# Performance work log

Measured on AMD Instinct MI355X. Metric: run time of the kernel, lower is better.

The kernel has to match this reference:

```python
import jax, jax.numpy as jnp
import numpy as np

C = 256
RED = 8
D = C // RED  # qk dim = 32
EPS = 1e-5   # nn.LayerNorm default


def setup_inputs() -> dict:
    key = jax.random.key(0)
    ks = jax.random.split(key, 10)
    B, H, W = 4, 64, 64
    s = 0.02
    return {
        "x": jax.random.normal(ks[0], (B, C, H, W), dtype=jnp.float32),
        "wq": jax.random.normal(ks[1], (D, C), dtype=jnp.float32) * s,
        "bq": jax.random.normal(ks[2], (D,), dtype=jnp.float32) * s,
        "wk": jax.random.normal(ks[3], (D, C), dtype=jnp.float32) * s,
        "bk": jax.random.normal(ks[4], (D,), dtype=jnp.float32) * s,
        "wv": jax.random.normal(ks[5], (C, C), dtype=jnp.float32) * s,
        "bv": jax.random.normal(ks[6], (C,), dtype=jnp.float32) * s,
        "gamma": jax.random.normal(ks[7], (1,), dtype=jnp.float32) * 0.1,
        "ln_w": jnp.ones((C,), dtype=jnp.float32),
        "ln_b": jnp.zeros((C,), dtype=jnp.float32),
    }


def reference(x, wq, bq, wk, bk, wv, bv, gamma, ln_w, ln_b):
    B, Cc, H, W = x.shape
    N = H * W
    xf = x.reshape(B, Cc, N)  # [B,C,N]
    # 1x1 convs == per-pixel linear over channels
    q = jnp.einsum('dc,bcn->bnd', wq, xf) + bq              # [B,N,D]
    k = jnp.einsum('dc,bcn->bdn', wk, xf) + bk[:, None]     # [B,D,N]
    v = jnp.einsum('ec,bcn->ben', wv, xf) + bv[:, None]     # [B,C,N]
    scale = 1.0 / (D ** 0.5)
    scores = jnp.einsum('bnd,bdm->bnm', q, k) * scale       # [B,N,N]
    # original subtracts row max then softmax; jax.nn.softmax is equivalent & stable
    attn = jax.nn.softmax(scores, axis=-1)                  # [B,N,N]
    out = jnp.einsum('bcm,bnm->bcn', v, attn)               # [B,C,N]
    res = gamma[0] * out + xf                               # gamma residual
    # LayerNorm over channel dim (module permutes to channels-last)
    r = res.transpose(0, 2, 1)                              # [B,N,C]
    mu = jnp.mean(r, axis=-1, keepdims=True)
    var = jnp.mean(jnp.square(r - mu), axis=-1, keepdims=True)
    y = (r - mu) * jax.lax.rsqrt(var + EPS) * ln_w + ln_b
    return y.transpose(0, 2, 1).reshape(B, Cc, H, W)
```

## Files before the change

kernel.cpp:

```cpp
#include <hip/hip_runtime.h>
#include <hip/hip_bf16.h>

#define NPIX 4096
#define NCH  256

typedef __attribute__((ext_vector_type(8))) short short8;
typedef __attribute__((ext_vector_type(16))) float f32x16;
typedef __attribute__((ext_vector_type(2))) unsigned int u32x2;

__device__ inline unsigned short bfbits(float f) {
    __hip_bfloat16 h = __float2bfloat16(f);
    return *reinterpret_cast<unsigned short*>(&h);
}

__device__ inline unsigned int pkfp8x4(float a, float b, float c, float d) {
    int w = __builtin_amdgcn_cvt_pk_fp8_f32(a, b, 0, false);
    w = __builtin_amdgcn_cvt_pk_fp8_f32(c, d, w, true);
    return (unsigned int)w;
}

__device__ inline unsigned char fp8b(float a) {
    return (unsigned char)(__builtin_amdgcn_cvt_pk_fp8_f32(a, a, 0, false) & 0xff);
}

__device__ inline float bperm(int srclane, float v) {
    return __int_as_float(__builtin_amdgcn_ds_bpermute(
        srclane << 2, __float_as_int(v)));
}

__global__ void __launch_bounds__(256) prep_kernel(
    const float* __restrict__ x,
    const float* __restrict__ wq, const float* __restrict__ bq,
    const float* __restrict__ wk, const float* __restrict__ bk,
    const float* __restrict__ wv, const float* __restrict__ bv,
    __hip_bfloat16* __restrict__ Wc, float* __restrict__ bc,
    __hip_bfloat16* __restrict__ XTg)
{
    const int bid = blockIdx.x;
    const int t   = threadIdx.x;
    if (bid >= 1024) {
        const int j = bid - 1024;
        const float kQ = 0.17677669529663687f * 1.4426950408889634f;
        const float* src;
        float sc = 1.0f;
        if (j < 32)       { src = wq + j * 256; }
        else if (j < 64)  { src = wk + (j - 32) * 256; sc = kQ; }
        else              { src = wv + (j - 64) * 256; }
        Wc[j * 256 + t] = __float2bfloat16(src[t] * sc);
        if (t == 0) {
            float bb = (j < 32) ? bq[j] : (j < 64) ? bk[j - 32] * kQ : bv[j - 64];
            bc[j] = bb;
        }
        return;
    }
    __shared__ float xs[64][65];
    const int b  = bid >> 8;
    const int c0 = ((bid >> 6) & 3) * 64;
    const int n0 = (bid & 63) * 64;
    const float* xb = x + ((size_t)b * NCH + c0) * NPIX + n0;
    #pragma unroll 4
    for (int i = 0; i < 16; ++i) {
        int c = i * 4 + (t >> 6);
        int n = t & 63;
        xs[c][n] = xb[(size_t)c * NPIX + n];
    }
    __syncthreads();
    #pragma unroll 4
    for (int i = 0; i < 16; ++i) {
        int nn = i * 4 + (t >> 6);
        int cL = t & 63;
        XTg[((size_t)b * NPIX + n0 + nn) * NCH + c0 + cL] =
            __float2bfloat16(xs[cL][nn]);
    }
}

__global__ void __launch_bounds__(256) proj_kernel(
    const __hip_bfloat16* __restrict__ Wc, const float* __restrict__ bc,
    const __hip_bfloat16* __restrict__ XTg,
    unsigned char* __restrict__ Q8, unsigned char* __restrict__ K8,
    unsigned char* __restrict__ V8)
{
    const int b    = blockIdx.z;
    const int t    = threadIdx.x;
    const int lane = t & 63;
    const int wid  = t >> 6;
    const int lo   = lane & 31;
    const int hi   = lane >> 5;
    const int n0   = blockIdx.x * 128 + wid * 32;
    const int jb   = blockIdx.y * 5;

    short8 xf[16];
    const __hip_bfloat16* xr = XTg + ((size_t)b * NPIX + n0 + lo) * NCH;
    #pragma unroll
    for (int ks = 0; ks < 16; ++ks)
        xf[ks] = *(const short8*)(xr + ks * 16 + hi * 8);

    for (int jo = 0; jo < 5; ++jo) {
        const int jt = jb + jo;
        f32x16 acc;
        #pragma unroll
        for (int r = 0; r < 16; ++r) acc[r] = 0.f;
        const __hip_bfloat16* wr = Wc + (size_t)(jt * 32 + lo) * NCH;
        #pragma unroll
        for (int ks = 0; ks < 16; ++ks) {
            short8 wf = *(const short8*)(wr + ks * 16 + hi * 8);
            acc = __builtin_amdgcn_mfma_f32_32x32x16_bf16(wf, xf[ks], acc, 0, 0, 0);
        }
        if (jt < 2) {
            unsigned char* dst = (jt == 0 ? Q8 : K8)
                               + ((size_t)b * NPIX + n0 + lo) * 32;
            #pragma unroll
            for (int g = 0; g < 4; ++g) {
                int jr = 8 * g + 4 * hi;
                unsigned int w = pkfp8x4(acc[4 * g + 0] + bc[jt * 32 + jr + 0],
                                         acc[4 * g + 1] + bc[jt * 32 + jr + 1],
                                         acc[4 * g + 2] + bc[jt * 32 + jr + 2],
                                         acc[4 * g + 3] + bc[jt * 32 + jr + 3]);
                *(unsigned int*)(dst + jr) = w;
            }
        } else {
            unsigned char* vb = V8 + (size_t)b * NPIX * NCH
                              + (size_t)((n0 + lo) >> 4) * 4096 + (lo & 15);
            #pragma unroll
            for (int r = 0; r < 16; ++r) {
                int jr = (r & 3) + 8 * (r >> 2) + 4 * hi;
                int c  = jt * 32 + jr - 64;
                vb[(size_t)c * 16] = fp8b(acc[r] + bc[jt * 32 + jr]);
            }
        }
    }
}

__global__ void __launch_bounds__(512, 4) attn_kernel(
    const unsigned char* __restrict__ Q8, const unsigned char* __restrict__ K8,
    const unsigned char* __restrict__ V8, const __hip_bfloat16* __restrict__ XTg,
    const float* __restrict__ gamma_p, const float* __restrict__ lnw,
    const float* __restrict__ lnb, float* __restrict__ out)
{
    __shared__ char smem[39936];

    const int t    = threadIdx.x;
    const int lane = t & 63;
    const int wid  = t >> 6;
    const int lo   = lane & 31;
    const int hi   = lane >> 5;

    const int lid = blockIdx.y * 128 + blockIdx.x;
    const int xcd = lid & 7;
    const int b   = xcd >> 1;
    const int q0  = ((xcd & 1) * 64 + (lid >> 3)) * 32;

    const unsigned char* Qb = Q8 + ((size_t)b * NPIX + q0) * 32;
    const long qf0 = *(const long*)(Qb + lo * 32 + hi * 8);
    const long qf1 = *(const long*)(Qb + lo * 32 + 16 + hi * 8);

    const unsigned char* Kw = K8 + (size_t)b * NPIX * 32
                            + (size_t)(wid * 32 + lo) * 32 + hi * 8;
    const unsigned char* Vw = V8 + (size_t)b * NPIX * NCH
                            + (size_t)(32 * wid + lo) * 16 + hi * 8;

    f32x16 acc;
    #pragma unroll
    for (int r = 0; r < 16; ++r) acc[r] = 0.f;
    float s_run = 0.f;

    long kA0 = *(const long*)(Kw);
    long kA1 = *(const long*)(Kw + 16);
    long kB0 = kA0, kB1 = kA1;

    const int swz = lo & 15;

    for (int it = 0; it < 16; ++it) {
        long vv[16];
        const unsigned char* vit = Vw + (size_t)(it * 16) * 4096;
        #pragma unroll
        for (int s = 0; s < 16; ++s)
            vv[s] = *(const long*)(vit + (size_t)s * 4096);

        if (it < 15) {
            kB0 = *(const long*)(Kw + (size_t)(it + 1) * 8192);
            kB1 = *(const long*)(Kw + (size_t)(it + 1) * 8192 + 16);
        }

        f32x16 sct;
        #pragma unroll
        for (int r = 0; r < 16; ++r) sct[r] = 0.f;
        sct = __builtin_amdgcn_mfma_f32_32x32x16_fp8_fp8(kA0, qf0, sct, 0, 0, 0);
        sct = __builtin_amdgcn_mfma_f32_32x32x16_fp8_fp8(kA1, qf1, sct, 0, 0, 0);

        char* pb = smem + (it & 1) * 8192 + lo * 256 + 4 * hi;
        float psum = 0.f;
        #pragma unroll
        for (int g = 0; g < 4; ++g) {
            float e0 = __builtin_exp2f(sct[4 * g + 0]);
            float e1 = __builtin_exp2f(sct[4 * g + 1]);
            float e2 = __builtin_exp2f(sct[4 * g + 2]);
            float e3 = __builtin_exp2f(sct[4 * g + 3]);
            psum += (e0 + e1) + (e2 + e3);
            unsigned int w = pkfp8x4(e0, e1, e2, e3);
            int gran = (4 * wid + g) ^ swz;
            *(unsigned int*)(pb + gran * 8) = w;
        }
        psum += __shfl_xor(psum, 32);
        s_run += psum;

        __syncthreads();

        const char* pr = smem + (it & 1) * 8192 + lo * 256;
        __builtin_amdgcn_s_setprio(1);
        #pragma unroll
        for (int s = 0; s < 16; ++s) {
            int gran = (2 * s + hi) ^ swz;
            long pa = *(const long*)(pr + gran * 8);
            acc = __builtin_amdgcn_mfma_f32_32x32x16_fp8_fp8(pa, vv[s], acc, 0, 0, 0);
        }
        __builtin_amdgcn_s_setprio(0);
        kA0 = kB0; kA1 = kB1;
    }

    float* red_sp = (float*)(smem + 36864);
    float* red2p  = (float*)(smem + 37888);
    float (*ybuf)[36] = (float(*)[36])smem;

    if (hi == 0) red_sp[wid * 32 + lo] = s_run;
    __syncthreads();
    float stot = 0.f;
    #pragma unroll
    for (int w = 0; w < 8; ++w) stot += red_sp[w * 32 + lo];
    const float invs = 1.0f / stot;
    const float gamma = gamma_p[0];
    const int cL = 32 * wid + lo;
    const __hip_bfloat16* XTb = XTg + ((size_t)b * NPIX + q0) * NCH + cL;
    float rv[16];
    #pragma unroll
    for (int r = 0; r < 16; ++r) {
        int qr = (r & 3) + 8 * (r >> 2) + 4 * hi;
        float ir = bperm(qr, invs);
        float xv = __bfloat162float(XTb[(size_t)qr * NCH]);
        rv[r] = gamma * (acc[r] * ir) + xv;
        float s1 = rv[r];
        float s2 = rv[r] * rv[r];
        #pragma unroll
        for (int off = 1; off < 32; off <<= 1) {
            s1 += __shfl_xor(s1, off);
            s2 += __shfl_xor(s2, off);
        }
        if (lo == 0) {
            red2p[qr * 16 + wid * 2]     = s1;
            red2p[qr * 16 + wid * 2 + 1] = s2;
        }
    }
    __syncthreads();
    float sA = 0.f, sB = 0.f;
    #pragma unroll
    for (int w = 0; w < 8; ++w) {
        sA += red2p[lo * 16 + w * 2];
        sB += red2p[lo * 16 + w * 2 + 1];
    }
    const float mean = sA * (1.f / 256.f);
    const float var  = sB * (1.f / 256.f) - mean * mean;
    const float rstd = rsqrtf(var + 1e-5f);
    const float lwv = lnw[cL];
    const float lbv = lnb[cL];
    #pragma unroll
    for (int r = 0; r < 16; ++r) {
        int qr = (r & 3) + 8 * (r >> 2) + 4 * hi;
        float m  = bperm(qr, mean);
        float rr = bperm(qr, rstd);
        ybuf[cL][qr] = (rv[r] - m) * rr * lwv + lbv;
    }
    __syncthreads();
    const int c_r = t >> 1;
    const int qh  = (t & 1) * 16;
    float* dst = out + ((size_t)b * NCH + c_r) * NPIX + q0 + qh;
    #pragma unroll
    for (int j = 0; j < 4; ++j) {
        float4 v;
        v.x = ybuf[c_r][qh + j * 4 + 0];
        v.y = ybuf[c_r][qh + j * 4 + 1];
        v.z = ybuf[c_r][qh + j * 4 + 2];
        v.w = ybuf[c_r][qh + j * 4 + 3];
        *(float4*)(dst + j * 4) = v;
    }
}

extern "C" void kernel_launch(void* const* d_in, const int* in_sizes, int n_in,
                              void* d_out, int out_size, void* d_ws, size_t ws_size,
                              hipStream_t stream) {
    const float* x     = (const float*)d_in[0];
    const float* wq    = (const float*)d_in[1];
    const float* bq    = (const float*)d_in[2];
    const float* wk    = (const float*)d_in[3];
    const float* bk    = (const float*)d_in[4];
    const float* wv    = (const float*)d_in[5];
    const float* bv    = (const float*)d_in[6];
    const float* gamma = (const float*)d_in[7];
    const float* ln_w  = (const float*)d_in[8];
    const float* ln_b  = (const float*)d_in[9];
    float* out = (float*)d_out;

    const int B = 4;
    unsigned char* ws = (unsigned char*)d_ws;
    unsigned char*  Q8 = ws;
    unsigned char*  K8 = ws + (512u << 10);
    unsigned char*  V8 = ws + (1u << 20);
    __hip_bfloat16* XT = (__hip_bfloat16*)(ws + (5u << 20));
    __hip_bfloat16* Wc = (__hip_bfloat16*)(ws + (13u << 20));
    float*          bc = (float*)(ws + (13u << 20) + 163840);

    prep_kernel<<<dim3(1344), 256, 0, stream>>>(x, wq, bq, wk, bk, wv, bv,
                                                Wc, bc, XT);
    proj_kernel<<<dim3(32, 2, B), 256, 0, stream>>>(Wc, bc, XT, Q8, K8, V8);
    attn_kernel<<<dim3(128, B), 512, 0, stream>>>(Q8, K8, V8, XT, gamma,
                                                  ln_w, ln_b, out);
}
```

Before: 94.34 us.

## Use scaled 32x32x64 FP8 MFMA in attention and merge projection grid

Replaces the pairs and quads of 32x32x16 FP8 MFMAs in the attention loop with single gfx950 scaled 32x32x64 f8f6f4 MFMAs, using unit scales (0x7F exponent) and packing four 8-byte fragments per operand. For QK^T, the 32-deep product is zero-padded to 64, wasting half of that instruction. The projection kernel now loops over all 10 output tiles per block instead of splitting them across two blocks in grid y. This halves the projection grid and lowers its parallelism, but reuses the loaded X fragments across all tiles.

```diff
diff --git a/kernel.cpp b/kernel.cpp
--- a/kernel.cpp
+++ b/kernel.cpp
@@ -7,6 +7,11 @@
 typedef __attribute__((ext_vector_type(8))) short short8;
 typedef __attribute__((ext_vector_type(16))) float f32x16;
 typedef __attribute__((ext_vector_type(2))) unsigned int u32x2;
+typedef __attribute__((ext_vector_type(8))) int i32x8;
+
+union Frag64 { long l[4]; i32x8 v; };
+
+#define SC1 0x7F7F7F7F
 
 __device__ inline unsigned short bfbits(float f) {
     __hip_bfloat16 h = __float2bfloat16(f);
@@ -87,7 +92,6 @@
     const int lo   = lane & 31;
     const int hi   = lane >> 5;
     const int n0   = blockIdx.x * 128 + wid * 32;
-    const int jb   = blockIdx.y * 5;
 
     short8 xf[16];
     const __hip_bfloat16* xr = XTg + ((size_t)b * NPIX + n0 + lo) * NCH;
@@ -95,8 +99,7 @@
     for (int ks = 0; ks < 16; ++ks)
         xf[ks] = *(const short8*)(xr + ks * 16 + hi * 8);
 
-    for (int jo = 0; jo < 5; ++jo) {
-        const int jt = jb + jo;
+    for (int jt = 0; jt < 10; ++jt) {
         f32x16 acc;
         #pragma unroll
         for (int r = 0; r < 16; ++r) acc[r] = 0.f;
@@ -151,8 +154,10 @@
     const int q0  = ((xcd & 1) * 64 + (lid >> 3)) * 32;
 
     const unsigned char* Qb = Q8 + ((size_t)b * NPIX + q0) * 32;
-    const long qf0 = *(const long*)(Qb + lo * 32 + hi * 8);
-    const long qf1 = *(const long*)(Qb + lo * 32 + 16 + hi * 8);
+    Frag64 qv;
+    qv.l[0] = *(const long*)(Qb + lo * 32 + hi * 8);
+    qv.l[1] = *(const long*)(Qb + lo * 32 + 16 + hi * 8);
+    qv.l[2] = 0; qv.l[3] = 0;
 
     const unsigned char* Kw = K8 + (size_t)b * NPIX * 32
                             + (size_t)(wid * 32 + lo) * 32 + hi * 8;
@@ -162,6 +167,9 @@
     f32x16 acc;
     #pragma unroll
     for (int r = 0; r < 16; ++r) acc[r] = 0.f;
+    f32x16 z16;
+    #pragma unroll
+    for (int r = 0; r < 16; ++r) z16[r] = 0.f;
     float s_run = 0.f;
 
     long kA0 = *(const long*)(Kw);
@@ -182,11 +190,10 @@
             kB1 = *(const long*)(Kw + (size_t)(it + 1) * 8192 + 16);
         }
 
-        f32x16 sct;
-        #pragma unroll
-        for (int r = 0; r < 16; ++r) sct[r] = 0.f;
-        sct = __builtin_amdgcn_mfma_f32_32x32x16_fp8_fp8(kA0, qf0, sct, 0, 0, 0);
-        sct = __builtin_amdgcn_mfma_f32_32x32x16_fp8_fp8(kA1, qf1, sct, 0, 0, 0);
+        Frag64 ka;
+        ka.l[0] = kA0; ka.l[1] = kA1; ka.l[2] = 0; ka.l[3] = 0;
+        f32x16 sct = __builtin_amdgcn_mfma_scale_f32_32x32x64_f8f6f4(
+            ka.v, qv.v, z16, 0, 0, 0, SC1, 0, SC1);
 
         char* pb = smem + (it & 1) * 8192 + lo * 256 + 4 * hi;
         float psum = 0.f;
@@ -209,10 +216,16 @@
         const char* pr = smem + (it & 1) * 8192 + lo * 256;
         __builtin_amdgcn_s_setprio(1);
         #pragma unroll
-        for (int s = 0; s < 16; ++s) {
-            int gran = (2 * s + hi) ^ swz;
-            long pa = *(const long*)(pr + gran * 8);
-            acc = __builtin_amdgcn_mfma_f32_32x32x16_fp8_fp8(pa, vv[s], acc, 0, 0, 0);
+        for (int s = 0; s < 4; ++s) {
+            Frag64 pa, vb;
+            #pragma unroll
+            for (int p = 0; p < 4; ++p) {
+                int gran = (8 * s + 2 * p + hi) ^ swz;
+                pa.l[p] = *(const long*)(pr + gran * 8);
+                vb.l[p] = vv[4 * s + p];
+            }
+            acc = __builtin_amdgcn_mfma_scale_f32_32x32x64_f8f6f4(
+                pa.v, vb.v, acc, 0, 0, 0, SC1, 0, SC1);
         }
         __builtin_amdgcn_s_setprio(0);
         kA0 = kB0; kA1 = kB1;
@@ -310,7 +323,7 @@
 
     prep_kernel<<<dim3(1344), 256, 0, stream>>>(x, wq, bq, wk, bk, wv, bv,
                                                 Wc, bc, XT);
-    proj_kernel<<<dim3(32, 2, B), 256, 0, stream>>>(Wc, bc, XT, Q8, K8, V8);
+    proj_kernel<<<dim3(32, 1, B), 256, 0, stream>>>(Wc, bc, XT, Q8, K8, V8);
     attn_kernel<<<dim3(128, B), 512, 0, stream>>>(Q8, K8, V8, XT, gamma,
                                                   ln_w, ln_b, out);
 }
```

New measurement: 104.2 us. +10.4%, slower.

## Split keys across waves and use scaled 32x32x64 fp8 MFMA with register P

Applied to the files above, without the earlier changes.

Restructures the attention kernel so each of four waves handles its own quarter of the key sequence and all 256 channels, instead of eight waves sharing keys and splitting channels. The P tile stays in registers, rearranged with v_permlane32_swap, rather than going through shared memory each iteration, which removes the per-iteration barrier. The PV product uses the wider scaled f8f6f4 32x32x64 MFMA. Per-wave partial outputs are merged in shared memory with atomicAdd before the LayerNorm. The cost is a large register footprint (eight f32x16 accumulators plus V fragments), fewer threads per block, and LDS atomic contention in the reduction.

```diff
diff --git a/kernel.cpp b/kernel.cpp
--- a/kernel.cpp
+++ b/kernel.cpp
@@ -6,12 +6,11 @@
 
 typedef __attribute__((ext_vector_type(8))) short short8;
 typedef __attribute__((ext_vector_type(16))) float f32x16;
-typedef __attribute__((ext_vector_type(2))) unsigned int u32x2;
-
-__device__ inline unsigned short bfbits(float f) {
-    __hip_bfloat16 h = __float2bfloat16(f);
-    return *reinterpret_cast<unsigned short*>(&h);
-}
+typedef __attribute__((ext_vector_type(8))) int i32x8;
+
+union Frag64 { long l[4]; i32x8 v; };
+
+#define SC1 0x7F7F7F7F
 
 __device__ inline unsigned int pkfp8x4(float a, float b, float c, float d) {
     int w = __builtin_amdgcn_cvt_pk_fp8_f32(a, b, 0, false);
@@ -131,13 +130,13 @@
     }
 }
 
-__global__ void __launch_bounds__(512, 4) attn_kernel(
+__global__ void __launch_bounds__(256, 2) attn_kernel(
     const unsigned char* __restrict__ Q8, const unsigned char* __restrict__ K8,
     const unsigned char* __restrict__ V8, const __hip_bfloat16* __restrict__ XTg,
     const float* __restrict__ gamma_p, const float* __restrict__ lnw,
     const float* __restrict__ lnb, float* __restrict__ out)
 {
-    __shared__ char smem[39936];
+    __shared__ char smem[39424];
 
     const int t    = threadIdx.x;
     const int lane = t & 63;
@@ -150,136 +149,171 @@
     const int b   = xcd >> 1;
     const int q0  = ((xcd & 1) * 64 + (lid >> 3)) * 32;
 
+    float4* ob4 = (float4*)smem;
+    float4 zz; zz.x = 0.f; zz.y = 0.f; zz.z = 0.f; zz.w = 0.f;
+    #pragma unroll
+    for (int i = 0; i < 8; ++i) ob4[t + 256 * i] = zz;
+
     const unsigned char* Qb = Q8 + ((size_t)b * NPIX + q0) * 32;
     const long qf0 = *(const long*)(Qb + lo * 32 + hi * 8);
     const long qf1 = *(const long*)(Qb + lo * 32 + 16 + hi * 8);
 
-    const unsigned char* Kw = K8 + (size_t)b * NPIX * 32
-                            + (size_t)(wid * 32 + lo) * 32 + hi * 8;
-    const unsigned char* Vw = V8 + (size_t)b * NPIX * NCH
-                            + (size_t)(32 * wid + lo) * 16 + hi * 8;
-
-    f32x16 acc;
-    #pragma unroll
-    for (int r = 0; r < 16; ++r) acc[r] = 0.f;
+    const unsigned char* Kp = K8 + (size_t)b * NPIX * 32
+                            + ((size_t)wid * 1024 + lo) * 32 + hi * 8;
+    const unsigned char* vbase = V8 + (size_t)b * NPIX * NCH
+                               + ((size_t)wid * 64) * 4096 + lo * 16 + hi * 8;
+    const unsigned char* vp0 = vbase;
+    const unsigned char* vp1 = vbase + 4096;
+    const unsigned char* vp2 = vbase + 8192;
+    const unsigned char* vp3 = vbase + 12288;
+
+    f32x16 acc[8];
+    #pragma unroll
+    for (int cb = 0; cb < 8; ++cb)
+        #pragma unroll
+        for (int r = 0; r < 16; ++r) acc[cb][r] = 0.f;
+    f32x16 z16;
+    #pragma unroll
+    for (int r = 0; r < 16; ++r) z16[r] = 0.f;
     float s_run = 0.f;
 
-    long kA0 = *(const long*)(Kw);
-    long kA1 = *(const long*)(Kw + 16);
-    long kB0 = kA0, kB1 = kA1;
-
-    const int swz = lo & 15;
-
-    for (int it = 0; it < 16; ++it) {
-        long vv[16];
-        const unsigned char* vit = Vw + (size_t)(it * 16) * 4096;
-        #pragma unroll
-        for (int s = 0; s < 16; ++s)
-            vv[s] = *(const long*)(vit + (size_t)s * 4096);
-
-        if (it < 15) {
-            kB0 = *(const long*)(Kw + (size_t)(it + 1) * 8192);
-            kB1 = *(const long*)(Kw + (size_t)(it + 1) * 8192 + 16);
-        }
-
-        f32x16 sct;
-        #pragma unroll
-        for (int r = 0; r < 16; ++r) sct[r] = 0.f;
-        sct = __builtin_amdgcn_mfma_f32_32x32x16_fp8_fp8(kA0, qf0, sct, 0, 0, 0);
-        sct = __builtin_amdgcn_mfma_f32_32x32x16_fp8_fp8(kA1, qf1, sct, 0, 0, 0);
-
-        char* pb = smem + (it & 1) * 8192 + lo * 256 + 4 * hi;
+    __syncthreads();
+
+    for (int ch = 0; ch < 16; ++ch) {
+        long kA0a = *(const long*)(Kp);
+        long kA1a = *(const long*)(Kp + 16);
+        long kA0b = *(const long*)(Kp + 1024);
+        long kA1b = *(const long*)(Kp + 1024 + 16);
+        Kp += 2048;
+
+        Frag64 vb[8];
+        #pragma unroll
+        for (int cb = 0; cb < 8; ++cb) {
+            vb[cb].l[0] = *(const long*)(vp0 + cb * 512);
+            vb[cb].l[1] = *(const long*)(vp1 + cb * 512);
+            vb[cb].l[2] = *(const long*)(vp2 + cb * 512);
+            vb[cb].l[3] = *(const long*)(vp3 + cb * 512);
+        }
+        vp0 += 16384; vp1 += 16384; vp2 += 16384; vp3 += 16384;
+
+        f32x16 s0 = __builtin_amdgcn_mfma_f32_32x32x16_fp8_fp8(kA0a, qf0, z16, 0, 0, 0);
+        s0 = __builtin_amdgcn_mfma_f32_32x32x16_fp8_fp8(kA1a, qf1, s0, 0, 0, 0);
+        f32x16 s1 = __builtin_amdgcn_mfma_f32_32x32x16_fp8_fp8(kA0b, qf0, z16, 0, 0, 0);
+        s1 = __builtin_amdgcn_mfma_f32_32x32x16_fp8_fp8(kA1b, qf1, s1, 0, 0, 0);
+
+        Frag64 pa;
         float psum = 0.f;
-        #pragma unroll
-        for (int g = 0; g < 4; ++g) {
-            float e0 = __builtin_exp2f(sct[4 * g + 0]);
-            float e1 = __builtin_exp2f(sct[4 * g + 1]);
-            float e2 = __builtin_exp2f(sct[4 * g + 2]);
-            float e3 = __builtin_exp2f(sct[4 * g + 3]);
-            psum += (e0 + e1) + (e2 + e3);
-            unsigned int w = pkfp8x4(e0, e1, e2, e3);
-            int gran = (4 * wid + g) ^ swz;
-            *(unsigned int*)(pb + gran * 8) = w;
-        }
-        psum += __shfl_xor(psum, 32);
+        {
+            float e[16];
+            #pragma unroll
+            for (int r = 0; r < 16; ++r) { e[r] = __builtin_exp2f(s0[r]); psum += e[r]; }
+            unsigned int X  = pkfp8x4(e[0], e[1], e[2], e[3]);
+            unsigned int Y  = pkfp8x4(e[4], e[5], e[6], e[7]);
+            asm("v_permlane32_swap_b32 %0, %1" : "+v"(X), "+v"(Y));
+            pa.l[0] = (long)(((unsigned long)Y << 32) | X);
+            unsigned int X2 = pkfp8x4(e[8], e[9], e[10], e[11]);
+            unsigned int Y2 = pkfp8x4(e[12], e[13], e[14], e[15]);
+            asm("v_permlane32_swap_b32 %0, %1" : "+v"(X2), "+v"(Y2));
+            pa.l[1] = (long)(((unsigned long)Y2 << 32) | X2);
+        }
+        {
+            float e[16];
+            #pragma unroll
+            for (int r = 0; r < 16; ++r) { e[r] = __builtin_exp2f(s1[r]); psum += e[r]; }
+            unsigned int X  = pkfp8x4(e[0], e[1], e[2], e[3]);
+            unsigned int Y  = pkfp8x4(e[4], e[5], e[6], e[7]);
+            asm("v_permlane32_swap_b32 %0, %1" : "+v"(X), "+v"(Y));
+            pa.l[2] = (long)(((unsigned long)Y << 32) | X);
+            unsigned int X2 = pkfp8x4(e[8], e[9], e[10], e[11]);
+            unsigned int Y2 = pkfp8x4(e[12], e[13], e[14], e[15]);
+            asm("v_permlane32_swap_b32 %0, %1" : "+v"(X2), "+v"(Y2));
+            pa.l[3] = (long)(((unsigned long)Y2 << 32) | X2);
+        }
         s_run += psum;
 
-        __syncthreads();
-
-        const char* pr = smem + (it & 1) * 8192 + lo * 256;
         __builtin_amdgcn_s_setprio(1);
         #pragma unroll
-        for (int s = 0; s < 16; ++s) {
-            int gran = (2 * s + hi) ^ swz;
-            long pa = *(const long*)(pr + gran * 8);
-            acc = __builtin_amdgcn_mfma_f32_32x32x16_fp8_fp8(pa, vv[s], acc, 0, 0, 0);
-        }
+        for (int cb = 0; cb < 8; ++cb)
+            acc[cb] = __builtin_amdgcn_mfma_scale_f32_32x32x64_f8f6f4(
+                pa.v, vb[cb].v, acc[cb], 0, 0, 0, SC1, 0, SC1);
         __builtin_amdgcn_s_setprio(0);
-        kA0 = kB0; kA1 = kB1;
-    }
-
-    float* red_sp = (float*)(smem + 36864);
-    float* red2p  = (float*)(smem + 37888);
-    float (*ybuf)[36] = (float(*)[36])smem;
-
+    }
+
+    float* ob     = (float*)smem;
+    float* red_sp = (float*)(smem + 37888);
+    float* red2p  = (float*)(smem + 38400);
+
+    #pragma unroll
+    for (int cb = 0; cb < 8; ++cb) {
+        #pragma unroll
+        for (int r = 0; r < 16; ++r) {
+            int qr = (r & 3) + 8 * (r >> 2) + 4 * hi;
+            atomicAdd(&ob[qr * 256 + 32 * cb + lo], acc[cb][r]);
+        }
+    }
+    s_run += __shfl_xor(s_run, 32);
     if (hi == 0) red_sp[wid * 32 + lo] = s_run;
     __syncthreads();
-    float stot = 0.f;
-    #pragma unroll
-    for (int w = 0; w < 8; ++w) stot += red_sp[w * 32 + lo];
+
+    float stot = red_sp[lo] + red_sp[32 + lo] + red_sp[64 + lo] + red_sp[96 + lo];
     const float invs = 1.0f / stot;
     const float gamma = gamma_p[0];
-    const int cL = 32 * wid + lo;
-    const __hip_bfloat16* XTb = XTg + ((size_t)b * NPIX + q0) * NCH + cL;
-    float rv[16];
+    const int cL0 = 32 * wid + lo;
+    const int cL1 = cL0 + 128;
+    const __hip_bfloat16* XTb = XTg + ((size_t)b * NPIX + q0) * NCH;
+    float rv[2][16];
     #pragma unroll
     for (int r = 0; r < 16; ++r) {
         int qr = (r & 3) + 8 * (r >> 2) + 4 * hi;
         float ir = bperm(qr, invs);
-        float xv = __bfloat162float(XTb[(size_t)qr * NCH]);
-        rv[r] = gamma * (acc[r] * ir) + xv;
-        float s1 = rv[r];
-        float s2 = rv[r] * rv[r];
+        float o0 = ob[qr * 256 + cL0];
+        float o1 = ob[qr * 256 + cL1];
+        float x0 = __bfloat162float(XTb[(size_t)qr * NCH + cL0]);
+        float x1 = __bfloat162float(XTb[(size_t)qr * NCH + cL1]);
+        rv[0][r] = gamma * (o0 * ir) + x0;
+        rv[1][r] = gamma * (o1 * ir) + x1;
+        float s1v = rv[0][r] + rv[1][r];
+        float s2v = rv[0][r] * rv[0][r] + rv[1][r] * rv[1][r];
         #pragma unroll
         for (int off = 1; off < 32; off <<= 1) {
-            s1 += __shfl_xor(s1, off);
-            s2 += __shfl_xor(s2, off);
+            s1v += __shfl_xor(s1v, off);
+            s2v += __shfl_xor(s2v, off);
         }
         if (lo == 0) {
-            red2p[qr * 16 + wid * 2]     = s1;
-            red2p[qr * 16 + wid * 2 + 1] = s2;
+            red2p[qr * 8 + wid * 2]     = s1v;
+            red2p[qr * 8 + wid * 2 + 1] = s2v;
         }
     }
     __syncthreads();
     float sA = 0.f, sB = 0.f;
     #pragma unroll
-    for (int w = 0; w < 8; ++w) {
-        sA += red2p[lo * 16 + w * 2];
-        sB += red2p[lo * 16 + w * 2 + 1];
+    for (int w = 0; w < 4; ++w) {
+        sA += red2p[lo * 8 + w * 2];
+        sB += red2p[lo * 8 + w * 2 + 1];
     }
     const float mean = sA * (1.f / 256.f);
     const float var  = sB * (1.f / 256.f) - mean * mean;
     const float rstd = rsqrtf(var + 1e-5f);
-    const float lwv = lnw[cL];
-    const float lbv = lnb[cL];
+    const float lw0 = lnw[cL0], lb0 = lnb[cL0];
+    const float lw1 = lnw[cL1], lb1 = lnb[cL1];
+    float (*ybuf)[37] = (float(*)[37])smem;
     #pragma unroll
     for (int r = 0; r < 16; ++r) {
         int qr = (r & 3) + 8 * (r >> 2) + 4 * hi;
         float m  = bperm(qr, mean);
         float rr = bperm(qr, rstd);
-        ybuf[cL][qr] = (rv[r] - m) * rr * lwv + lbv;
-    }
-    __syncthreads();
-    const int c_r = t >> 1;
-    const int qh  = (t & 1) * 16;
-    float* dst = out + ((size_t)b * NCH + c_r) * NPIX + q0 + qh;
-    #pragma unroll
-    for (int j = 0; j < 4; ++j) {
+        ybuf[cL0][qr] = (rv[0][r] - m) * rr * lw0 + lb0;
+        ybuf[cL1][qr] = (rv[1][r] - m) * rr * lw1 + lb1;
+    }
+    __syncthreads();
+    float* dst = out + ((size_t)b * NCH + t) * NPIX + q0;
+    #pragma unroll
+    for (int j = 0; j < 8; ++j) {
         float4 v;
-        v.x = ybuf[c_r][qh + j * 4 + 0];
-        v.y = ybuf[c_r][qh + j * 4 + 1];
-        v.z = ybuf[c_r][qh + j * 4 + 2];
-        v.w = ybuf[c_r][qh + j * 4 + 3];
+        v.x = ybuf[t][j * 4 + 0];
+        v.y = ybuf[t][j * 4 + 1];
+        v.z = ybuf[t][j * 4 + 2];
+        v.w = ybuf[t][j * 4 + 3];
         *(float4*)(dst + j * 4) = v;
     }
 }
@@ -311,6 +345,6 @@
     prep_kernel<<<dim3(1344), 256, 0, stream>>>(x, wq, bq, wk, bk, wv, bv,
                                                 Wc, bc, XT);
     proj_kernel<<<dim3(32, 2, B), 256, 0, stream>>>(Wc, bc, XT, Q8, K8, V8);
-    attn_kernel<<<dim3(128, B), 512, 0, stream>>>(Q8, K8, V8, XT, gamma,
+    attn_kernel<<<dim3(128, B), 256, 0, stream>>>(Q8, K8, V8, XT, gamma,
                                                   ln_w, ln_b, out);
 }
```

Result: slower. 160.5 us (+70.2%).
